# Performance work log

Measured on AMD Instinct MI355X. Metric: run time of the kernel, lower is better.

Reference implementation:

```python
import jax, jax.numpy as jnp
import numpy as np

# Geometry constants fixed by the source's index arithmetic
GRID_P, GRID_Q, NUM_ANCH = 60, 40, 9   # p = (i//9)%60, q = i//(60*9), sr = i%9
N = GRID_P * GRID_Q * NUM_ANCH          # 21600 anchors per image
K = 1000                                # top-K candidates kept before NMS
MAX_BOXES = 18                          # fixed output boxes per image
THRESH = 0.5                            # NMS overlap threshold
BATCH = 64


def setup_inputs() -> dict:
    key = jax.random.key(0)
    k1, k2 = jax.random.split(key)
    x = jax.random.normal(k1, (BATCH, N, 6), dtype=jnp.float32)
    # anchor boxes (x, y, w, h); keep w,h strictly positive and away from 0
    anchor_boxes = jax.random.uniform(k2, (GRID_P, GRID_Q, NUM_ANCH, 4),
                                      dtype=jnp.float32, minval=0.05, maxval=1.0)
    return {"x": x, "anchor_boxes": anchor_boxes}


def _per_sample(ypred, anchors):
    scores, order = jax.lax.top_k(ypred[:, 0], K)          # descending, matches tf.argsort DESC [:1000]
    p = (order // NUM_ANCH) % GRID_P
    q = order // (GRID_P * NUM_ANCH)
    sr = order % NUM_ANCH
    a = anchors[p, q, sr]                                   # [K, 4] (xa, ya, wa, ha)
    regr = ypred[order, 2:6]                                # [K, 4] (dx, dy, dw, dh)
    xc = regr[:, 0] * a[:, 2] + a[:, 0]
    yc = regr[:, 1] * a[:, 3] + a[:, 1]
    w = a[:, 2] * jnp.exp(regr[:, 2])
    h = a[:, 3] * jnp.exp(regr[:, 3])
    cand = jnp.stack([xc, yc, w, h, scores], axis=-1)       # [K, 5] xywh+score

    # xywh -> xyxy for overlap computation (as in non_max_suppression_fast)
    x1 = xc - 0.5 * w; x2 = xc + 0.5 * w
    y1 = yc - 0.5 * h; y2 = yc + 0.5 * h
    area = (x2 - x1) * (y2 - y1)                            # [K]

    # pairwise intersection; overlap[i, j] = inter(i, j) / area(j)  (source divides by
    # the area of the lower-scored candidate, NOT the union -- kept faithfully)
    xx1 = jnp.maximum(x1[:, None], x1[None, :])
    yy1 = jnp.maximum(y1[:, None], y1[None, :])
    xx2 = jnp.minimum(x2[:, None], x2[None, :])
    yy2 = jnp.minimum(y2[:, None], y2[None, :])
    iw = jnp.maximum(0.0, xx2 - xx1)
    ih = jnp.maximum(0.0, yy2 - yy1)
    sup = (iw * ih / area[None, :]) > THRESH                # [K, K] bool

    # greedy NMS over candidates in descending-score order
    jrange = jnp.arange(K)
    def body(i, keep):
        return keep & ~(keep[i] & sup[i] & (jrange > i))
    keep = jax.lax.fori_loop(0, K, body, jnp.ones((K,), dtype=bool))

    # pack first MAX_BOXES kept boxes into fixed-shape output
    ranks = jnp.cumsum(keep) - 1                            # position among kept
    valid = keep & (ranks < MAX_BOXES)
    picked = jnp.zeros((MAX_BOXES, 5), cand.dtype).at[
        jnp.where(valid, ranks, MAX_BOXES)
    ].set(jnp.where(valid[:, None], cand, 0.0), mode='drop')

    # pad with top-scored decoded boxes if fewer than MAX_BOXES survive NMS
    n = jnp.minimum(jnp.sum(keep), MAX_BOXES)
    j = jnp.arange(MAX_BOXES)
    pad = cand[jnp.clip(j - n, 0, K - 1)]
    return jnp.where((j < n)[:, None], picked, pad)         # [MAX_BOXES, 5]


def reference(x, anchor_boxes):
    return jax.vmap(lambda y: _per_sample(y, anchor_boxes))(x)  # [B, 18, 5]
```

## Files before the change

### kernel.cpp

```cpp
#include <hip/hip_runtime.h>

#define NELEM 21600
#define KSEL 1000
#define MAXB 18
#define NT 1024
#define CAP 2048
#define NCHUNK 8
#define QC 4050
#define NFULL 21
#define NTAIL (NELEM - NFULL * NT)

typedef unsigned long long ull;

__device__ __forceinline__ unsigned fkey(float f) {
  unsigned u = __float_as_uint(f);
  return (u & 0x80000000u) ? ~u : (u | 0x80000000u);
}
__device__ __forceinline__ float unfkey(unsigned k) {
  unsigned u = (k & 0x80000000u) ? (k ^ 0x80000000u) : ~k;
  return __uint_as_float(u);
}

#define K1PROC(v, g) { int r = (g) % 3; \
  if (r == 0) { unsigned key = fkey((v).x); gk[2 * ((g) / 3)] = key; atomicAdd(&h[key >> 21], 1u); } \
  else if (r == 1) { unsigned key = fkey((v).z); gk[2 * ((g) / 3) + 1] = key; atomicAdd(&h[key >> 21], 1u); } }

__global__ __launch_bounds__(NT) void k1_scan(
    const float* __restrict__ x, unsigned* __restrict__ gkeys,
    unsigned* __restrict__ ghist) {
  const int blk = blockIdx.x;
  const int s = blk / NCHUNK, c = blk % NCHUNK;
  const int t = threadIdx.x;
  const float4* xq = (const float4*)(x + (size_t)s * NELEM * 6);
  unsigned* gk = gkeys + (size_t)s * NELEM;

  __shared__ unsigned h[2048];
  h[2 * t] = 0u; h[2 * t + 1] = 0u;

  const int base = c * QC;
  float4 va0 = xq[base + t];
  float4 va1 = xq[base + t + 1024];
  float4 va2 = xq[base + t + 2048];
  const bool hast = t < (QC - 3072);
  float4 vt = hast ? xq[base + t + 3072] : va0;
  asm volatile("" :
      "+v"(va0.x), "+v"(va0.y), "+v"(va0.z), "+v"(va0.w),
      "+v"(va1.x), "+v"(va1.y), "+v"(va1.z), "+v"(va1.w),
      "+v"(va2.x), "+v"(va2.y), "+v"(va2.z), "+v"(va2.w),
      "+v"(vt.x), "+v"(vt.y), "+v"(vt.z), "+v"(vt.w));
  __syncthreads();

  { int g = base + t;        K1PROC(va0, g) }
  { int g = base + t + 1024; K1PROC(va1, g) }
  { int g = base + t + 2048; K1PROC(va2, g) }
  if (hast) { int g = base + t + 3072; K1PROC(vt, g) }
  __syncthreads();
  unsigned* gh = ghist + (size_t)blk * 2048;
  gh[2 * t] = h[2 * t];
  gh[2 * t + 1] = h[2 * t + 1];
}

__device__ void select_bucket(const unsigned* hist, unsigned target,
                              volatile unsigned* chunkSuf,
                              unsigned* outB, unsigned* outCnt, unsigned* outAbove) {
  const int tid = threadIdx.x;
  const int w = tid >> 6, l = tid & 63;
  unsigned h1 = hist[w * 128 + 2 * l + 1];
  unsigned s = hist[w * 128 + 2 * l] + h1;
  #pragma unroll
  for (int d = 1; d < 64; d <<= 1) {
    unsigned t = __shfl_down(s, d);
    if (l + d < 64) s += t;
  }
  if (l == 0) chunkSuf[w] = s;
  __syncthreads();
  if (w == 0) {
    unsigned ct = (l < 16) ? chunkSuf[l] : 0u;
    unsigned cs = ct;
    #pragma unroll
    for (int d = 1; d < 16; d <<= 1) {
      unsigned t = __shfl_down(cs, d);
      if (l + d < 16) cs += t;
    }
    if (l < 16) chunkSuf[l] = cs - ct;
  }
  __syncthreads();
  unsigned base = chunkSuf[w];
  unsigned sufE = s + base;
  unsigned sN = __shfl_down(s, 1);
  unsigned sufN = ((l < 63) ? sN : 0u) + base;
  unsigned geOdd = sufN + h1;
  if (sufE >= target && geOdd < target) { *outB = w * 128u + 2u * l;     *outCnt = sufE;  *outAbove = geOdd; }
  if (geOdd >= target && sufN < target) { *outB = w * 128u + 2u * l + 1; *outCnt = geOdd; *outAbove = sufN;  }
  __syncthreads();
}

__global__ __launch_bounds__(NT, 4) void k2_main(
    const float* __restrict__ x, const float* __restrict__ anch,
    const unsigned* __restrict__ gkeys, const unsigned* __restrict__ ghist,
    float* __restrict__ out) {
  const int s = blockIdx.x;
  const int tid = threadIdx.x;
  const float* xb = x + (size_t)s * NELEM * 6;
  const unsigned* ks = gkeys + (size_t)s * NELEM;

  __shared__ unsigned hist[2048];
  __shared__ unsigned chunkSuf[16];
  __shared__ ull selPk[CAP];
  __shared__ float px1[1088], py1[1088], px2[1088], py2[1088];
  __shared__ unsigned sB, sCnt, sAbove;
  __shared__ unsigned baseKey, cnt;
  __shared__ int keptRank[MAXB];
  __shared__ int numKept;

  unsigned kv[NFULL];
  #pragma unroll
  for (int u = 0; u < NFULL; ++u) kv[u] = ks[tid + (u << 10)];
  unsigned ktail = 0u;
  const bool hastail = tid < NTAIL;
  if (hastail) ktail = ks[tid + NFULL * NT];

  {
    unsigned h0 = 0, h1 = 0;
    #pragma unroll
    for (int c = 0; c < NCHUNK; ++c) {
      const unsigned* gh = ghist + (size_t)(s * NCHUNK + c) * 2048;
      h0 += gh[2 * tid];
      h1 += gh[2 * tid + 1];
    }
    hist[2 * tid] = h0; hist[2 * tid + 1] = h1;
  }
  __syncthreads();
  select_bucket(hist, KSEL, chunkSuf, &sB, &sCnt, &sAbove);
  const unsigned b1 = sB, cnt1 = sCnt, above1 = sAbove;

  asm volatile("" :
      "+v"(kv[0]), "+v"(kv[1]), "+v"(kv[2]), "+v"(kv[3]), "+v"(kv[4]),
      "+v"(kv[5]), "+v"(kv[6]), "+v"(kv[7]), "+v"(kv[8]), "+v"(kv[9]),
      "+v"(kv[10]), "+v"(kv[11]), "+v"(kv[12]), "+v"(kv[13]), "+v"(kv[14]),
      "+v"(kv[15]), "+v"(kv[16]), "+v"(kv[17]), "+v"(kv[18]), "+v"(kv[19]),
      "+v"(kv[20]), "+v"(ktail));

  if (cnt1 > 1024) {
    hist[2 * tid] = 0u; hist[2 * tid + 1] = 0u;
    __syncthreads();
    #pragma unroll
    for (int u = 0; u < NFULL; ++u)
      if ((kv[u] >> 21) == b1) atomicAdd(&hist[(kv[u] >> 10) & 0x7FFu], 1u);
    if (hastail && (ktail >> 21) == b1) atomicAdd(&hist[(ktail >> 10) & 0x7FFu], 1u);
    __syncthreads();
    select_bucket(hist, KSEL - above1, chunkSuf, &sB, &sCnt, &sAbove);
    if (tid == 0) { baseKey = (b1 << 21) | (sB << 10); cnt = 0u; }
  } else {
    if (tid == 0) { baseKey = b1 << 21; cnt = 0u; }
  }
  __syncthreads();

  {
    const unsigned TB = baseKey;
    const int lw = tid & 63;
    #pragma unroll
    for (int u = 0; u < NFULL; ++u) {
      bool pred = kv[u] >= TB;
      ull mask = __ballot(pred);
      if (mask) {
        int leader = __builtin_ctzll(mask);
        unsigned total = (unsigned)__popcll(mask);
        unsigned basep = 0;
        if (lw == leader) basep = atomicAdd(&cnt, total);
        basep = __shfl(basep, leader);
        if (pred) {
          unsigned p = basep + (unsigned)__popcll(mask & ((1ull << lw) - 1ull));
          unsigned i = (unsigned)(tid + (u << 10));
          if (p < CAP) selPk[p] = ((ull)kv[u] << 32) | (unsigned)(~i);
        }
      }
    }
    if (hastail && ktail >= TB) {
      unsigned p = atomicAdd(&cnt, 1u);
      unsigned i = (unsigned)(tid + NFULL * NT);
      if (p < CAP) selPk[p] = ((ull)ktail << 32) | (unsigned)(~i);
    }
  }
  __syncthreads();
  const unsigned cntS = (cnt < CAP) ? cnt : CAP;
  const unsigned P = (cntS <= 1024u) ? 1024u : 2048u;
  for (unsigned i = cntS + tid; i < P; i += NT) selPk[i] = 0ull;
  __syncthreads();

  if (P == 1024u) {
    ull a = selPk[tid];
    #pragma unroll
    for (unsigned k = 2; k <= 64; k <<= 1) {
      #pragma unroll
      for (unsigned j = k >> 1; j >= 1; j >>= 1) {
        bool up = ((tid & k) == 0);
        bool lower = ((tid & j) == 0);
        bool takeMax = (up == lower);
        ull o = __shfl_xor(a, (int)j);
        a = takeMax ? (a > o ? a : o) : (a < o ? a : o);
      }
    }
    selPk[tid] = a;
    __syncthreads();
    for (unsigned k = 128; k <= 1024; k <<= 1) {
      for (unsigned j = k >> 1; j >= 64; j >>= 1) {
        if (tid < 512) {
          unsigned p = (unsigned)tid;
          unsigned vi = ((p & ~(j - 1)) << 1) | (p & (j - 1));
          unsigned li = vi | j;
          ull av = selPk[vi], cv = selPk[li];
          bool doswap = ((vi & k) == 0) ? (av < cv) : (av > cv);
          if (doswap) { selPk[vi] = cv; selPk[li] = av; }
        }
        __syncthreads();
      }
      a = selPk[tid];
      {
        bool up = ((tid & k) == 0);
        #pragma unroll
        for (unsigned j = 32; j >= 1; j >>= 1) {
          bool lower = ((tid & j) == 0);
          bool takeMax = (up == lower);
          ull o = __shfl_xor(a, (int)j);
          a = takeMax ? (a > o ? a : o) : (a < o ? a : o);
        }
      }
      selPk[tid] = a;
      __syncthreads();
    }
  } else {
    const int w = tid >> 6, L = tid & 63;
    const int ea = (w << 7) | (L << 1);
    ull a = selPk[ea], bb = selPk[ea + 1];
    #pragma unroll
    for (unsigned k = 2; k <= 128; k <<= 1) {
      #pragma unroll
      for (unsigned j = k >> 1; j >= 2; j >>= 1) {
        bool up = ((ea & k) == 0);
        bool lower = ((ea & j) == 0);
        bool takeMax = (up == lower);
        ull oa = __shfl_xor(a, (int)(j >> 1));
        ull ob = __shfl_xor(bb, (int)(j >> 1));
        a  = takeMax ? (a  > oa ? a  : oa) : (a  < oa ? a  : oa);
        bb = takeMax ? (bb > ob ? bb : ob) : (bb < ob ? bb : ob);
      }
      bool up = ((ea & k) == 0);
      ull mx = a > bb ? a : bb, mn = a > bb ? bb : a;
      a = up ? mx : mn; bb = up ? mn : mx;
    }
    selPk[ea] = a; selPk[ea + 1] = bb;
    __syncthreads();
    for (unsigned k = 256; k <= 2048; k <<= 1) {
      for (unsigned j = k >> 1; j >= 128; j >>= 1) {
        unsigned p = (unsigned)tid;
        unsigned vi = ((p & ~(j - 1)) << 1) | (p & (j - 1));
        unsigned li = vi | j;
        ull av = selPk[vi], cv = selPk[li];
        bool doswap = ((vi & k) == 0) ? (av < cv) : (av > cv);
        if (doswap) { selPk[vi] = cv; selPk[li] = av; }
        __syncthreads();
      }
      a = selPk[ea]; bb = selPk[ea + 1];
      bool up = (((unsigned)(w << 7) & k) == 0);
      #pragma unroll
      for (unsigned j = 64; j >= 2; j >>= 1) {
        bool lower = ((ea & j) == 0);
        bool takeMax = (up == lower);
        ull oa = __shfl_xor(a, (int)(j >> 1));
        ull ob = __shfl_xor(bb, (int)(j >> 1));
        a  = takeMax ? (a  > oa ? a  : oa) : (a  < oa ? a  : oa);
        bb = takeMax ? (bb > ob ? bb : ob) : (bb < ob ? bb : ob);
      }
      ull mx = a > bb ? a : bb, mn = a > bb ? bb : a;
      a = up ? mx : mn; bb = up ? mn : mx;
      selPk[ea] = a; selPk[ea + 1] = bb;
      __syncthreads();
    }
  }

  if (tid < KSEL) {
    unsigned idx = ~(unsigned)selPk[tid];
    const float2* e2 = (const float2*)(xb + (size_t)idx * 6 + 2);
    float2 ra = e2[0], rb = e2[1];
    unsigned pp = (idx / 9u) % 60u;
    unsigned qq = idx / 540u;
    unsigned sr = idx % 9u;
    const float* ap = anch + (((pp * 40u + qq) * 9u + sr) * 4u);
    float ax = ap[0], ay = ap[1], aw = ap[2], ah = ap[3];
    float xc = ra.x * aw + ax;
    float yc = ra.y * ah + ay;
    float w = aw * expf(rb.x);
    float h = ah * expf(rb.y);
    int a = (tid >> 4) * 17 + (tid & 15);
    px1[a] = xc - 0.5f * w; px2[a] = xc + 0.5f * w;
    py1[a] = yc - 0.5f * h; py2[a] = yc + 0.5f * h;
  }
  __syncthreads();

  if (tid < 64) {
    const int lane = tid;
    unsigned alive = 0u;
    #pragma unroll
    for (int ss = 0; ss < 16; ++ss) {
      int r = lane * 16 + ss;
      alive |= (r < KSEL ? 1u : 0u) << ss;
    }
    int nk = 0;
    while (nk < MAXB) {
      ull bal = __ballot(alive != 0u);
      if (!bal) break;
      int F = __builtin_ctzll(bal);
      int myss = (int)__builtin_ctz(alive | 0x10000u);
      int ssw = __shfl(myss, F);
      int m = F * 16 + ssw;
      if (lane == 0) keptRank[nk] = m;
      int am = (m >> 4) * 17 + (m & 15);
      float wx1 = px1[am], wy1 = py1[am], wx2 = px2[am], wy2 = py2[am];
      ++nk;
      if (nk >= MAXB) break;
      #pragma unroll
      for (int ss = 0; ss < 16; ++ss) {
        if (alive & (1u << ss)) {
          int a = lane * 17 + ss;
          float x1 = px1[a], y1 = py1[a], x2 = px2[a], y2 = py2[a];
          float iw = fmaxf(fminf(x2, wx2) - fmaxf(x1, wx1), 0.f);
          float ih = fmaxf(fminf(y2, wy2) - fmaxf(y1, wy1), 0.f);
          float ar = (x2 - x1) * (y2 - y1);
          if (iw * ih / ar > 0.5f) alive &= ~(1u << ss);
        }
      }
    }
    if (lane == 0) numKept = nk;
  }
  __syncthreads();

  const int n = numKept;
  if (tid < MAXB) {
    int j = tid;
    int r = (j < n) ? keptRank[j] : (j - n);
    ull pk = selPk[r];
    unsigned idx = ~(unsigned)pk;
    float sc = unfkey((unsigned)(pk >> 32));
    const float2* e2 = (const float2*)(xb + (size_t)idx * 6 + 2);
    float2 ra = e2[0], rb = e2[1];
    unsigned pp = (idx / 9u) % 60u;
    unsigned qq = idx / 540u;
    unsigned sr = idx % 9u;
    const float* ap = anch + (((pp * 40u + qq) * 9u + sr) * 4u);
    float ax = ap[0], ay = ap[1], aw = ap[2], ah = ap[3];
    float xc = ra.x * aw + ax;
    float yc = ra.y * ah + ay;
    float w = aw * expf(rb.x);
    float h = ah * expf(rb.y);
    float* o = out + s * (MAXB * 5) + j * 5;
    o[0] = xc; o[1] = yc; o[2] = w; o[3] = h; o[4] = sc;
  }
}

extern "C" void kernel_launch(void* const* d_in, const int* in_sizes, int n_in,
                              void* d_out, int out_size, void* d_ws, size_t ws_size,
                              hipStream_t stream) {
  const float* x = (const float*)d_in[0];
  const float* anch = (const float*)d_in[1];
  float* out = (float*)d_out;
  const int B = in_sizes[0] / (NELEM * 6);
  unsigned* ghist = (unsigned*)d_ws;
  unsigned* gkeys = ghist + (size_t)B * NCHUNK * 2048;
  k1_scan<<<dim3(B * NCHUNK), dim3(NT), 0, stream>>>(x, gkeys, ghist);
  k2_main<<<dim3(B), dim3(NT), 0, stream>>>(x, anch, gkeys, ghist, out);
}
```

Baseline: 65.14 us.

## Split candidate compaction into a separate multi-block kernel per sample

Adds a middle kernel that uses four blocks per sample to threshold the keys by the first-level histogram bucket and compact them into a global per-sample buffer, with an atomic global counter. The final kernel loads that buffer, or falls back to a two-level refinement when the bucket overflows CAP. The sort always takes the 2048-element path, and the scan now uses four chunks per sample instead of eight. The goal is to spread the key scan across more blocks than one per sample. In exchange it adds a kernel launch and a global round-trip, drops the cheaper 1024-element sort, and gives the scan kernel fewer blocks.

```diff
diff --git a/kernel.cpp b/kernel.cpp
--- a/kernel.cpp
+++ b/kernel.cpp
@@ -5,8 +5,9 @@
 #define MAXB 18
 #define NT 1024
 #define CAP 2048
-#define NCHUNK 8
-#define QC 4050
+#define NCHUNK 4
+#define QC 8100
+#define QK 5400
 #define NFULL 21
 #define NTAIL (NELEM - NFULL * NT)
 
@@ -21,39 +22,40 @@
   return __uint_as_float(u);
 }
 
-#define K1PROC(v, g) { int r = (g) % 3; \
-  if (r == 0) { unsigned key = fkey((v).x); gk[2 * ((g) / 3)] = key; atomicAdd(&h[key >> 21], 1u); } \
-  else if (r == 1) { unsigned key = fkey((v).z); gk[2 * ((g) / 3) + 1] = key; atomicAdd(&h[key >> 21], 1u); } }
-
 __global__ __launch_bounds__(NT) void k1_scan(
     const float* __restrict__ x, unsigned* __restrict__ gkeys,
-    unsigned* __restrict__ ghist) {
+    unsigned* __restrict__ ghist, unsigned* __restrict__ gcnt,
+    unsigned* __restrict__ gflag) {
   const int blk = blockIdx.x;
-  const int s = blk / NCHUNK, c = blk % NCHUNK;
+  const int s = blk >> 2, c = blk & 3;
   const int t = threadIdx.x;
   const float4* xq = (const float4*)(x + (size_t)s * NELEM * 6);
   unsigned* gk = gkeys + (size_t)s * NELEM;
 
   __shared__ unsigned h[2048];
   h[2 * t] = 0u; h[2 * t + 1] = 0u;
+  if (c == 0 && t == 0) { gcnt[s] = 0u; gflag[s] = 0u; }
+  __syncthreads();
 
   const int base = c * QC;
-  float4 va0 = xq[base + t];
-  float4 va1 = xq[base + t + 1024];
-  float4 va2 = xq[base + t + 2048];
-  const bool hast = t < (QC - 3072);
-  float4 vt = hast ? xq[base + t + 3072] : va0;
-  asm volatile("" :
-      "+v"(va0.x), "+v"(va0.y), "+v"(va0.z), "+v"(va0.w),
-      "+v"(va1.x), "+v"(va1.y), "+v"(va1.z), "+v"(va1.w),
-      "+v"(va2.x), "+v"(va2.y), "+v"(va2.z), "+v"(va2.w),
-      "+v"(vt.x), "+v"(vt.y), "+v"(vt.z), "+v"(vt.w));
-  __syncthreads();
-
-  { int g = base + t;        K1PROC(va0, g) }
-  { int g = base + t + 1024; K1PROC(va1, g) }
-  { int g = base + t + 2048; K1PROC(va2, g) }
-  if (hast) { int g = base + t + 3072; K1PROC(vt, g) }
+  #pragma unroll
+  for (int k = 0; k < 8; ++k) {
+    int off = t + (k << 10);
+    if (k < 7 || off < QC) {
+      int g = base + off;
+      float4 v = xq[g];
+      int r = g % 3;
+      if (r == 0) {
+        unsigned key = fkey(v.x);
+        gk[2 * (g / 3)] = key;
+        atomicAdd(&h[key >> 21], 1u);
+      } else if (r == 1) {
+        unsigned key = fkey(v.z);
+        gk[2 * (g / 3) + 1] = key;
+        atomicAdd(&h[key >> 21], 1u);
+      }
+    }
+  }
   __syncthreads();
   unsigned* gh = ghist + (size_t)blk * 2048;
   gh[2 * t] = h[2 * t];
@@ -95,30 +97,19 @@
   __syncthreads();
 }
 
-__global__ __launch_bounds__(NT, 4) void k2_main(
-    const float* __restrict__ x, const float* __restrict__ anch,
+__global__ __launch_bounds__(NT) void k2_compact(
     const unsigned* __restrict__ gkeys, const unsigned* __restrict__ ghist,
-    float* __restrict__ out) {
-  const int s = blockIdx.x;
+    ull* __restrict__ gselPk, unsigned* __restrict__ gcnt,
+    unsigned* __restrict__ gflag) {
+  const int blk = blockIdx.x;
+  const int s = blk >> 2, q = blk & 3;
   const int tid = threadIdx.x;
-  const float* xb = x + (size_t)s * NELEM * 6;
-  const unsigned* ks = gkeys + (size_t)s * NELEM;
 
   __shared__ unsigned hist[2048];
   __shared__ unsigned chunkSuf[16];
-  __shared__ ull selPk[CAP];
-  __shared__ float px1[1088], py1[1088], px2[1088], py2[1088];
+  __shared__ ull lbuf[CAP];
+  __shared__ unsigned lcnt, gbase;
   __shared__ unsigned sB, sCnt, sAbove;
-  __shared__ unsigned baseKey, cnt;
-  __shared__ int keptRank[MAXB];
-  __shared__ int numKept;
-
-  unsigned kv[NFULL];
-  #pragma unroll
-  for (int u = 0; u < NFULL; ++u) kv[u] = ks[tid + (u << 10)];
-  unsigned ktail = 0u;
-  const bool hastail = tid < NTAIL;
-  if (hastail) ktail = ks[tid + NFULL * NT];
 
   {
     unsigned h0 = 0, h1 = 0;
@@ -130,18 +121,89 @@
     }
     hist[2 * tid] = h0; hist[2 * tid + 1] = h1;
   }
+  if (tid == 0) lcnt = 0u;
   __syncthreads();
   select_bucket(hist, KSEL, chunkSuf, &sB, &sCnt, &sAbove);
-  const unsigned b1 = sB, cnt1 = sCnt, above1 = sAbove;
-
-  asm volatile("" :
-      "+v"(kv[0]), "+v"(kv[1]), "+v"(kv[2]), "+v"(kv[3]), "+v"(kv[4]),
-      "+v"(kv[5]), "+v"(kv[6]), "+v"(kv[7]), "+v"(kv[8]), "+v"(kv[9]),
-      "+v"(kv[10]), "+v"(kv[11]), "+v"(kv[12]), "+v"(kv[13]), "+v"(kv[14]),
-      "+v"(kv[15]), "+v"(kv[16]), "+v"(kv[17]), "+v"(kv[18]), "+v"(kv[19]),
-      "+v"(kv[20]), "+v"(ktail));
-
-  if (cnt1 > 1024) {
+
+  if (sCnt > (unsigned)CAP) {
+    if (tid == 0 && q == 0) gflag[s] = 1u;
+    return;
+  }
+  const unsigned TB = sB << 21;
+  const unsigned* ks = gkeys + (size_t)s * NELEM + q * QK;
+  const int lw = tid & 63;
+  #pragma unroll
+  for (int it = 0; it < 6; ++it) {
+    int i = tid + (it << 10);
+    bool pred = false;
+    unsigned k = 0u;
+    if (i < QK) { k = ks[i]; pred = (k >= TB); }
+    ull mask = __ballot(pred);
+    if (mask) {
+      int leader = __builtin_ctzll(mask);
+      unsigned tot = (unsigned)__popcll(mask);
+      unsigned bp = 0;
+      if (lw == leader) bp = atomicAdd(&lcnt, tot);
+      bp = __shfl(bp, leader);
+      if (pred) {
+        unsigned p = bp + (unsigned)__popcll(mask & ((1ull << lw) - 1ull));
+        unsigned idx = (unsigned)(q * QK + i);
+        lbuf[p] = ((ull)k << 32) | (unsigned)(~idx);
+      }
+    }
+  }
+  __syncthreads();
+  if (tid == 0) gbase = atomicAdd(&gcnt[s], lcnt);
+  __syncthreads();
+  ull* gs = gselPk + (size_t)s * CAP;
+  const unsigned n = lcnt, b0 = gbase;
+  for (unsigned i = tid; i < n; i += NT) gs[b0 + i] = lbuf[i];
+}
+
+__global__ __launch_bounds__(NT, 4) void k3_final(
+    const float* __restrict__ x, const float* __restrict__ anch,
+    const unsigned* __restrict__ gkeys, const unsigned* __restrict__ ghist,
+    const ull* __restrict__ gselPk, const unsigned* __restrict__ gcnt,
+    const unsigned* __restrict__ gflag, float* __restrict__ out) {
+  const int s = blockIdx.x;
+  const int tid = threadIdx.x;
+  const float* xb = x + (size_t)s * NELEM * 6;
+
+  __shared__ ull selPk[CAP];
+  __shared__ float px1[1088], py1[1088], px2[1088], py2[1088];
+  __shared__ unsigned hist[2048];
+  __shared__ unsigned chunkSuf[16];
+  __shared__ unsigned sB, sCnt, sAbove;
+  __shared__ unsigned cnt;
+  __shared__ int keptRank[MAXB];
+  __shared__ int numKept;
+
+  if (gflag[s] == 0u) {
+    const unsigned n = gcnt[s];
+    const ull* gs = gselPk + (size_t)s * CAP;
+    for (unsigned i = tid; i < CAP; i += NT) selPk[i] = (i < n) ? gs[i] : 0ull;
+    __syncthreads();
+  } else {
+    const unsigned* ks = gkeys + (size_t)s * NELEM;
+    unsigned kv[NFULL];
+    #pragma unroll
+    for (int u = 0; u < NFULL; ++u) kv[u] = ks[tid + (u << 10)];
+    unsigned ktail = 0u;
+    const bool hastail = tid < NTAIL;
+    if (hastail) ktail = ks[tid + NFULL * NT];
+    {
+      unsigned h0 = 0, h1 = 0;
+      #pragma unroll
+      for (int c = 0; c < NCHUNK; ++c) {
+        const unsigned* gh = ghist + (size_t)(s * NCHUNK + c) * 2048;
+        h0 += gh[2 * tid];
+        h1 += gh[2 * tid + 1];
+      }
+      hist[2 * tid] = h0; hist[2 * tid + 1] = h1;
+    }
+    __syncthreads();
+    select_bucket(hist, KSEL, chunkSuf, &sB, &sCnt, &sAbove);
+    const unsigned b1 = sB, above1 = sAbove;
     hist[2 * tid] = 0u; hist[2 * tid + 1] = 0u;
     __syncthreads();
     #pragma unroll
@@ -150,14 +212,9 @@
     if (hastail && (ktail >> 21) == b1) atomicAdd(&hist[(ktail >> 10) & 0x7FFu], 1u);
     __syncthreads();
     select_bucket(hist, KSEL - above1, chunkSuf, &sB, &sCnt, &sAbove);
-    if (tid == 0) { baseKey = (b1 << 21) | (sB << 10); cnt = 0u; }
-  } else {
-    if (tid == 0) { baseKey = b1 << 21; cnt = 0u; }
-  }
-  __syncthreads();
-
-  {
-    const unsigned TB = baseKey;
+    const unsigned TB = (b1 << 21) | (sB << 10);
+    if (tid == 0) cnt = 0u;
+    __syncthreads();
     const int lw = tid & 63;
     #pragma unroll
     for (int u = 0; u < NFULL; ++u) {
@@ -181,55 +238,13 @@
       unsigned i = (unsigned)(tid + NFULL * NT);
       if (p < CAP) selPk[p] = ((ull)ktail << 32) | (unsigned)(~i);
     }
-  }
-  __syncthreads();
-  const unsigned cntS = (cnt < CAP) ? cnt : CAP;
-  const unsigned P = (cntS <= 1024u) ? 1024u : 2048u;
-  for (unsigned i = cntS + tid; i < P; i += NT) selPk[i] = 0ull;
-  __syncthreads();
-
-  if (P == 1024u) {
-    ull a = selPk[tid];
-    #pragma unroll
-    for (unsigned k = 2; k <= 64; k <<= 1) {
-      #pragma unroll
-      for (unsigned j = k >> 1; j >= 1; j >>= 1) {
-        bool up = ((tid & k) == 0);
-        bool lower = ((tid & j) == 0);
-        bool takeMax = (up == lower);
-        ull o = __shfl_xor(a, (int)j);
-        a = takeMax ? (a > o ? a : o) : (a < o ? a : o);
-      }
-    }
-    selPk[tid] = a;
-    __syncthreads();
-    for (unsigned k = 128; k <= 1024; k <<= 1) {
-      for (unsigned j = k >> 1; j >= 64; j >>= 1) {
-        if (tid < 512) {
-          unsigned p = (unsigned)tid;
-          unsigned vi = ((p & ~(j - 1)) << 1) | (p & (j - 1));
-          unsigned li = vi | j;
-          ull av = selPk[vi], cv = selPk[li];
-          bool doswap = ((vi & k) == 0) ? (av < cv) : (av > cv);
-          if (doswap) { selPk[vi] = cv; selPk[li] = av; }
-        }
-        __syncthreads();
-      }
-      a = selPk[tid];
-      {
-        bool up = ((tid & k) == 0);
-        #pragma unroll
-        for (unsigned j = 32; j >= 1; j >>= 1) {
-          bool lower = ((tid & j) == 0);
-          bool takeMax = (up == lower);
-          ull o = __shfl_xor(a, (int)j);
-          a = takeMax ? (a > o ? a : o) : (a < o ? a : o);
-        }
-      }
-      selPk[tid] = a;
-      __syncthreads();
-    }
-  } else {
+    __syncthreads();
+    const unsigned realCnt = (cnt < CAP) ? cnt : CAP;
+    for (unsigned i = realCnt + tid; i < CAP; i += NT) selPk[i] = 0ull;
+    __syncthreads();
+  }
+
+  {
     const int w = tid >> 6, L = tid & 63;
     const int ea = (w << 7) | (L << 1);
     ull a = selPk[ea], bb = selPk[ea + 1];
@@ -365,8 +380,12 @@
   const float* anch = (const float*)d_in[1];
   float* out = (float*)d_out;
   const int B = in_sizes[0] / (NELEM * 6);
-  unsigned* ghist = (unsigned*)d_ws;
+  ull* gselPk = (ull*)d_ws;
+  unsigned* ghist = (unsigned*)(gselPk + (size_t)B * CAP);
   unsigned* gkeys = ghist + (size_t)B * NCHUNK * 2048;
-  k1_scan<<<dim3(B * NCHUNK), dim3(NT), 0, stream>>>(x, gkeys, ghist);
-  k2_main<<<dim3(B), dim3(NT), 0, stream>>>(x, anch, gkeys, ghist, out);
-}
+  unsigned* gcnt = gkeys + (size_t)B * NELEM;
+  unsigned* gflag = gcnt + B;
+  k1_scan<<<dim3(B * NCHUNK), dim3(NT), 0, stream>>>(x, gkeys, ghist, gcnt, gflag);
+  k2_compact<<<dim3(B * NCHUNK), dim3(NT), 0, stream>>>(gkeys, ghist, gselPk, gcnt, gflag);
+  k3_final<<<dim3(B), dim3(NT), 0, stream>>>(x, anch, gkeys, ghist, gselPk, gcnt, gflag, out);
+}
```

After: 69.90 us. 7.3% more time.
